# Performance work log

Measured on AMD Instinct MI355X. Metric: run time of the kernel, lower is better.

The kernel has to match this reference:

```python
import jax, jax.numpy as jnp
import numpy as np

MD = 4                  # corr_md
D = 2 * MD + 1          # patch_size = 9


def setup_inputs() -> dict:
    key = jax.random.key(0)
    k1, k2 = jax.random.split(key)
    b, c, h, w = 4, 128, 128, 256
    t1 = jax.random.normal(k1, (b, c, h, w), dtype=jnp.float32)
    t2 = jax.random.normal(k2, (b, c, h, w), dtype=jnp.float32)
    return {"t1": t1, "t2": t2}


def reference(t1, t2):
    # Local cost volume: for each displacement (di, dj) in [-MD, MD]^2,
    # out[b, p, y, x] = sum_c t1[b, c, y, x] * t2[b, c, y+di, x+dj]
    # with zero padding outside t2 (SpatialCorrelationSampler semantics,
    # kernel_size=1, stride=1, dilation_patch=1; no channel normalization).
    b, c, h, w = t1.shape
    t2p = jnp.pad(t2, ((0, 0), (0, 0), (MD, MD), (MD, MD)))
    # Loop over the fixed 9x9 displacement grid (81 small reductions);
    outs = [
        jnp.einsum('bchw,bchw->bhw', t1, t2p[:, :, i:i + h, j:j + w])
        for i in range(D) for j in range(D)
    ]
    return jnp.stack(outs, axis=1)  # [b, 81, h, w]
```

## Files before the change

### kernel.cpp

```cpp
#include <hip/hip_runtime.h>

#define NP 81
#define CC 128
#define HH 128
#define WW 256
#define SX 24
#define NXT 11
#define NBLK (NXT * 16 * 4)
#define YPAD 136
#define XPAD 272
#define WS_NEED (4ull * YPAD * XPAD * CC * 2ull)

typedef __attribute__((ext_vector_type(8))) short short8;
typedef __attribute__((ext_vector_type(4))) float f32x4;
typedef __attribute__((ext_vector_type(16))) float f32x16;

__device__ __forceinline__ short f2bf(float f) {
    unsigned int u = __builtin_bit_cast(unsigned int, f);
    u += 0x7fffu + ((u >> 16) & 1u);
    return (short)(u >> 16);
}

__global__ __launch_bounds__(256) void prepass_t2t(const float* __restrict__ t2,
                                                   short* __restrict__ ws) {
    const int blk = blockIdx.x;
    const int yp  = blk % YPAD;
    const int b   = blk / YPAD;
    const int tid = threadIdx.x;
    short* wrow = ws + (size_t)blk * XPAD * CC;
    const int y2 = yp - 4;
    const short8 z = {0, 0, 0, 0, 0, 0, 0, 0};
    if (y2 < 0 || y2 >= HH) {
        for (int u = tid; u < XPAD * CC / 8; u += 256)
            *(short8*)&wrow[(size_t)u * 8] = z;
        return;
    }
    __shared__ short sT[64 * 136];
    {
        const int xh = tid >> 4;
        const int xp = (xh < 4) ? xh : xh + 256;
        *(short8*)&wrow[(size_t)xp * CC + (tid & 15) * 8] = z;
    }
    const int c   = tid & 127;
    const int x4h = tid >> 7;
    const int oct = tid & 15;
    const int xr  = tid >> 4;
    const float* prow = t2 + ((size_t)(b * CC + c) * HH + y2) * WW;
    for (int ch = 0; ch < 4; ++ch) {
        const int xbase = ch * 64;
#pragma unroll
        for (int rr = 0; rr < 8; ++rr) {
            const int x4 = x4h + 2 * rr;
            const f32x4 vv = *(const f32x4*)&prow[xbase + x4 * 4];
#pragma unroll
            for (int j = 0; j < 4; ++j)
                sT[(x4 * 4 + j) * 136 + c] = f2bf(vv[j]);
        }
        __syncthreads();
#pragma unroll
        for (int r2 = 0; r2 < 4; ++r2) {
            const int x = xr + 16 * r2;
            const short8 vv = *(const short8*)&sT[x * 136 + oct * 8];
            *(short8*)&wrow[(size_t)(xbase + x + 4) * CC + oct * 8] = vv;
        }
        __syncthreads();
    }
}

__global__ __launch_bounds__(1024) void corr_main24(
        const float* __restrict__ t1, const short* __restrict__ ws,
        float* __restrict__ out) {
    const int bid = blockIdx.x;
    const int sw  = (bid & 7) * (NBLK / 8) + (bid >> 3);
    const int ys = sw & 15;
    const int v  = sw >> 4;
    const int xt = v % NXT;
    const int b  = v / NXT;
    const int X0 = xt * SX;
    const int y0 = ys * 8;

    const int tid  = threadIdx.x;
    const int lane = tid & 63;
    const int w    = tid >> 6;
    const int n    = lane & 31;
    const int g    = lane >> 5;

    __shared__ short sA[8 * SX * 128];
    __shared__ __align__(16) float obufs[16 * 9 * 28];

    const short* bp = ws + ((size_t)(b * YPAD + y0 + w) * XPAD + X0 + n) * CC
                    + g * 8;
    short8 bre[8];
#pragma unroll
    for (int kc = 0; kc < 8; ++kc)
        bre[kc] = *(const short8*)&bp[kc * 16];

#pragma unroll
    for (int i = 0; i < 6; ++i) {
        const int idx = tid + i * 1024;
        const int x4 = idx % 6;
        const int vv = idx / 6;
        const int c  = vv & 127;
        const int yy = vv >> 7;
        const int xg = X0 + x4 * 4;
        f32x4 t = {0.f, 0.f, 0.f, 0.f};
        if (xg < WW)
            t = *(const f32x4*)&t1[((size_t)(b * CC + c) * HH + y0 + yy) * WW + xg];
        const int oct = c >> 3;
#pragma unroll
        for (int j = 0; j < 4; ++j) {
            const int x = x4 * 4 + j;
            sA[yy * 3072 + x * 128 + ((oct ^ (x & 15)) * 8 + (c & 7))] = f2bf(t[j]);
        }
    }
    __syncthreads();

    const int ylo = (w > 8) ? (w - 8) : 0;
    const int yhi = (w < 7) ? w : 7;
    float* ob = &obufs[w * 252];

    for (int yy = ylo; yy <= yhi; ++yy) {
        const int sbase = yy * 3072 + n * 128;

        f32x16 a;
#pragma unroll
        for (int q = 0; q < 16; ++q) a[q] = 0.f;
#pragma unroll
        for (int kc = 0; kc < 8; ++kc) {
            const short8 af = *(const short8*)
                &sA[sbase + (((kc * 2 + g) ^ (n & 15)) * 8)];
            a = __builtin_amdgcn_mfma_f32_32x32x16_bf16(af, bre[kc], a, 0, 0, 0);
        }

#pragma unroll
        for (int q = 0; q < 16; ++q) {
            const int m  = (q & 3) + 8 * (q >> 2) + 4 * g;
            const int dj = n - m;
            if (dj >= 0 && dj <= 8 && m < SX) ob[dj * 28 + m] = a[q];
        }

        const int di = w - yy;
        const int y  = y0 + yy;
        if (lane < 54) {
            const int dj = lane / 6, xq = lane % 6;
            if (X0 + xq * 4 < WW) {
                f32x4 vv = *(const f32x4*)&ob[dj * 28 + xq * 4];
                *(f32x4*)&out[((size_t)(b * NP + di * 9 + dj) * HH + y) * WW
                              + X0 + xq * 4] = vv;
            }
        }
    }
}

__global__ __launch_bounds__(1024) void corr_fallback(
        const float* __restrict__ t1, const float* __restrict__ t2,
        float* __restrict__ out) {
    const int bid = blockIdx.x;
    const int sw  = (bid & 7) * (NBLK / 8) + (bid >> 3);
    const int ys = sw & 15;
    const int v  = sw >> 4;
    const int xt = v % NXT;
    const int b  = v / NXT;
    const int X0 = xt * SX;
    const int y0 = ys * 8;
    const int tid  = threadIdx.x;
    const int lane = tid & 63;
    const int w    = tid >> 6;
    const int n    = lane & 31;
    const int g    = lane >> 5;
    __shared__ short sA[8 * SX * 128];
    __shared__ __align__(16) float obufs[16 * 9 * 28];
    const size_t plane = (size_t)HH * WW;
    const int r = y0 - 4 + w;
#pragma unroll
    for (int i = 0; i < 3; ++i) {
        const int unit = tid + i * 1024;
        const int x    = unit % SX;
        const int rest = unit / SX;
        const int oct  = rest & 15;
        const int yy   = rest >> 4;
        short8 pk = {0,0,0,0,0,0,0,0};
        if (X0 + x < WW) {
            const float* p = t1 + ((size_t)(b * CC + oct * 8) * HH + (y0 + yy)) * WW
                           + X0 + x;
#pragma unroll
            for (int j = 0; j < 8; ++j) pk[j] = f2bf(p[(size_t)j * plane]);
        }
        *(short8*)&sA[yy * (SX * 128) + x * 128 + ((oct ^ (x & 15)) * 8)] = pk;
    }
    __syncthreads();
    const int x2 = X0 - 4 + n;
    const bool ok = (r >= 0) && (r < HH) && (x2 >= 0) && (x2 < WW);
    const int rc  = r  < 0 ? 0 : (r  > HH - 1 ? HH - 1 : r);
    const int xc  = x2 < 0 ? 0 : (x2 > WW - 1 ? WW - 1 : x2);
    const float* bp = t2 + ((size_t)(b * CC + g * 8) * HH + rc) * WW + xc;
    short8 bre[8];
#pragma unroll
    for (int kc = 0; kc < 8; ++kc) {
        short8 f;
#pragma unroll
        for (int j = 0; j < 8; ++j) f[j] = f2bf(bp[(size_t)(kc * 16 + j) * plane]);
        if (!ok) f = (short8){0,0,0,0,0,0,0,0};
        bre[kc] = f;
    }
    const int ylo = (w > 8) ? (w - 8) : 0;
    const int yhi = (w < 7) ? w : 7;
    float* ob = &obufs[w * 252];
    for (int yy = ylo; yy <= yhi; ++yy) {
        const int sbase = yy * (SX * 128) + n * 128;
        f32x16 a;
#pragma unroll
        for (int q = 0; q < 16; ++q) a[q] = 0.f;
#pragma unroll
        for (int kc = 0; kc < 8; ++kc) {
            const short8 af = *(const short8*)
                &sA[sbase + (((kc * 2 + g) ^ (n & 15)) * 8)];
            a = __builtin_amdgcn_mfma_f32_32x32x16_bf16(af, bre[kc], a, 0, 0, 0);
        }
#pragma unroll
        for (int q = 0; q < 16; ++q) {
            const int m  = (q & 3) + 8 * (q >> 2) + 4 * g;
            const int dj = n - m;
            if (dj >= 0 && dj <= 8 && m < SX) ob[dj * 28 + m] = a[q];
        }
        const int di = w - yy;
        const int y  = y0 + yy;
        if (lane < 54) {
            const int dj = lane / 6, xq = lane % 6;
            if (X0 + xq * 4 < WW) {
                f32x4 vv = *(const f32x4*)&ob[dj * 28 + xq * 4];
                *(f32x4*)&out[((size_t)(b * NP + di * 9 + dj) * HH + y) * WW
                              + X0 + xq * 4] = vv;
            }
        }
    }
}

extern "C" void kernel_launch(void* const* d_in, const int* in_sizes, int n_in,
                              void* d_out, int out_size, void* d_ws, size_t ws_size,
                              hipStream_t stream) {
    const float* t1 = (const float*)d_in[0];
    const float* t2 = (const float*)d_in[1];
    if (ws_size >= WS_NEED) {
        short* ws = (short*)d_ws;
        prepass_t2t<<<4 * YPAD, 256, 0, stream>>>(t2, ws);
        corr_main24<<<NBLK, 1024, 0, stream>>>(t1, ws, (float*)d_out);
    } else {
        corr_fallback<<<NBLK, 1024, 0, stream>>>(t1, t2, (float*)d_out);
    }
}
```

Measured before the change: 210.2 us.

## Shrink x-tile to 16, split prepass in halves, vectorize channel-packed loads

The main kernel moves from 24-wide x tiles (11 tiles, the last one partial) to 16-wide tiles, so there are exactly 1024 blocks and no bounds checks. This drops the wasted partial tile and the padding lanes in the MFMA M dimension, at the cost of more redundant loads of the halo t2 data per output. The t2 prepass now runs two blocks per row, each handling half the channels. It loads 8 channel planes directly and packs them into bf16 short8 without a shared-memory transpose. The t1 staging is likewise rewritten so each thread packs four channels into bf16x4 stores.

```diff
diff --git a/kernel.cpp b/kernel.cpp
--- a/kernel.cpp
+++ b/kernel.cpp
@@ -4,13 +4,14 @@
 #define CC 128
 #define HH 128
 #define WW 256
-#define SX 24
-#define NXT 11
-#define NBLK (NXT * 16 * 4)
 #define YPAD 136
 #define XPAD 272
 #define WS_NEED (4ull * YPAD * XPAD * CC * 2ull)
 
+#define SX 16
+#define NBLK 1024
+
+typedef __attribute__((ext_vector_type(4))) short bf16x4;
 typedef __attribute__((ext_vector_type(8))) short short8;
 typedef __attribute__((ext_vector_type(4))) float f32x4;
 typedef __attribute__((ext_vector_type(16))) float f32x16;
@@ -24,58 +25,52 @@
 __global__ __launch_bounds__(256) void prepass_t2t(const float* __restrict__ t2,
                                                    short* __restrict__ ws) {
     const int blk = blockIdx.x;
-    const int yp  = blk % YPAD;
-    const int b   = blk / YPAD;
+    const int hf  = blk & 1;
+    const int row = blk >> 1;
+    const int yp  = row % YPAD;
+    const int b   = row / YPAD;
     const int tid = threadIdx.x;
-    short* wrow = ws + (size_t)blk * XPAD * CC;
+    short* wrow = ws + (size_t)row * XPAD * CC;
     const int y2 = yp - 4;
-    const short8 z = {0, 0, 0, 0, 0, 0, 0, 0};
+    const short8 z = {0,0,0,0,0,0,0,0};
     if (y2 < 0 || y2 >= HH) {
-        for (int u = tid; u < XPAD * CC / 8; u += 256)
+        for (int u = tid + hf * 2176; u < 2176 + hf * 2176; u += 256)
             *(short8*)&wrow[(size_t)u * 8] = z;
         return;
     }
-    __shared__ short sT[64 * 136];
-    {
-        const int xh = tid >> 4;
-        const int xp = (xh < 4) ? xh : xh + 256;
+    if (tid < 128) {
+        const int idx = hf * 8 + (tid >> 4);
+        const int xp  = (idx < 4) ? idx : idx + 256;
         *(short8*)&wrow[(size_t)xp * CC + (tid & 15) * 8] = z;
     }
-    const int c   = tid & 127;
-    const int x4h = tid >> 7;
-    const int oct = tid & 15;
-    const int xr  = tid >> 4;
-    const float* prow = t2 + ((size_t)(b * CC + c) * HH + y2) * WW;
-    for (int ch = 0; ch < 4; ++ch) {
-        const int xbase = ch * 64;
-#pragma unroll
-        for (int rr = 0; rr < 8; ++rr) {
-            const int x4 = x4h + 2 * rr;
-            const f32x4 vv = *(const f32x4*)&prow[xbase + x4 * 4];
-#pragma unroll
-            for (int j = 0; j < 4; ++j)
-                sT[(x4 * 4 + j) * 136 + c] = f2bf(vv[j]);
-        }
-        __syncthreads();
-#pragma unroll
-        for (int r2 = 0; r2 < 4; ++r2) {
-            const int x = xr + 16 * r2;
-            const short8 vv = *(const short8*)&sT[x * 136 + oct * 8];
-            *(short8*)&wrow[(size_t)(xbase + x + 4) * CC + oct * 8] = vv;
-        }
-        __syncthreads();
-    }
-}
-
-__global__ __launch_bounds__(1024) void corr_main24(
+    const size_t plane = (size_t)HH * WW;
+#pragma unroll
+    for (int i = 0; i < 2; ++i) {
+        const int u   = tid + i * 256;
+        const int oct = hf * 8 + (u & 7);
+        const int xq  = u >> 3;
+        const float* p = t2 + ((size_t)(b * CC + oct * 8) * HH + y2) * WW + xq * 4;
+        f32x4 v[8];
+#pragma unroll
+        for (int j = 0; j < 8; ++j) v[j] = *(const f32x4*)&p[(size_t)j * plane];
+#pragma unroll
+        for (int jj = 0; jj < 4; ++jj) {
+            short8 s;
+#pragma unroll
+            for (int j = 0; j < 8; ++j) s[j] = f2bf(v[j][jj]);
+            *(short8*)&wrow[(size_t)(4 + xq * 4 + jj) * CC + oct * 8] = s;
+        }
+    }
+}
+
+__global__ __launch_bounds__(1024) void corr_main16(
         const float* __restrict__ t1, const short* __restrict__ ws,
         float* __restrict__ out) {
     const int bid = blockIdx.x;
     const int sw  = (bid & 7) * (NBLK / 8) + (bid >> 3);
-    const int ys = sw & 15;
-    const int v  = sw >> 4;
-    const int xt = v % NXT;
-    const int b  = v / NXT;
+    const int xt = sw & 15;
+    const int ys = (sw >> 4) & 15;
+    const int b  = sw >> 8;
     const int X0 = xt * SX;
     const int y0 = ys * 8;
 
@@ -86,7 +81,7 @@
     const int g    = lane >> 5;
 
     __shared__ short sA[8 * SX * 128];
-    __shared__ __align__(16) float obufs[16 * 9 * 28];
+    __shared__ __align__(16) float obufs[16 * 9 * 20];
 
     const short* bp = ws + ((size_t)(b * YPAD + y0 + w) * XPAD + X0 + n) * CC
                     + g * 8;
@@ -95,32 +90,37 @@
     for (int kc = 0; kc < 8; ++kc)
         bre[kc] = *(const short8*)&bp[kc * 16];
 
-#pragma unroll
-    for (int i = 0; i < 6; ++i) {
-        const int idx = tid + i * 1024;
-        const int x4 = idx % 6;
-        const int vv = idx / 6;
-        const int c  = vv & 127;
-        const int yy = vv >> 7;
-        const int xg = X0 + x4 * 4;
-        f32x4 t = {0.f, 0.f, 0.f, 0.f};
-        if (xg < WW)
-            t = *(const f32x4*)&t1[((size_t)(b * CC + c) * HH + y0 + yy) * WW + xg];
-        const int oct = c >> 3;
-#pragma unroll
-        for (int j = 0; j < 4; ++j) {
-            const int x = x4 * 4 + j;
-            sA[yy * 3072 + x * 128 + ((oct ^ (x & 15)) * 8 + (c & 7))] = f2bf(t[j]);
+    if (tid < 512) {
+        const int oct = tid & 15;
+        const int xq  = (tid >> 4) & 3;
+        const int yy  = tid >> 6;
+        const size_t plane = (size_t)HH * WW;
+        const float* p = t1 + ((size_t)(b * CC + oct * 8) * HH + y0 + yy) * WW
+                       + X0 + xq * 4;
+#pragma unroll
+        for (int h = 0; h < 2; ++h) {
+            f32x4 v[4];
+#pragma unroll
+            for (int j = 0; j < 4; ++j)
+                v[j] = *(const f32x4*)&p[(size_t)(h * 4 + j) * plane];
+#pragma unroll
+            for (int jj = 0; jj < 4; ++jj) {
+                const int x = xq * 4 + jj;
+                bf16x4 s;
+#pragma unroll
+                for (int j = 0; j < 4; ++j) s[j] = f2bf(v[j][jj]);
+                *(bf16x4*)&sA[yy * 2048 + x * 128 + ((oct ^ x) * 8) + h * 4] = s;
+            }
         }
     }
     __syncthreads();
 
     const int ylo = (w > 8) ? (w - 8) : 0;
     const int yhi = (w < 7) ? w : 7;
-    float* ob = &obufs[w * 252];
+    float* ob = &obufs[w * 180];
 
     for (int yy = ylo; yy <= yhi; ++yy) {
-        const int sbase = yy * 3072 + n * 128;
+        const int sbase = yy * 2048 + n * 128;
 
         f32x16 a;
 #pragma unroll
@@ -136,9 +136,94 @@
         for (int q = 0; q < 16; ++q) {
             const int m  = (q & 3) + 8 * (q >> 2) + 4 * g;
             const int dj = n - m;
-            if (dj >= 0 && dj <= 8 && m < SX) ob[dj * 28 + m] = a[q];
-        }
-
+            if (dj >= 0 && dj <= 8 && m < SX) ob[dj * 20 + m] = a[q];
+        }
+
+        const int di = w - yy;
+        const int y  = y0 + yy;
+        if (lane < 36) {
+            const int dj = lane >> 2, xq = lane & 3;
+            f32x4 vv = *(const f32x4*)&ob[dj * 20 + xq * 4];
+            *(f32x4*)&out[((size_t)(b * NP + di * 9 + dj) * HH + y) * WW
+                          + X0 + xq * 4] = vv;
+        }
+    }
+}
+
+#define FB_SX 24
+#define FB_NXT 11
+#define FB_NBLK (FB_NXT * 16 * 4)
+__global__ __launch_bounds__(1024) void corr_fallback(
+        const float* __restrict__ t1, const float* __restrict__ t2,
+        float* __restrict__ out) {
+    const int bid = blockIdx.x;
+    const int sw  = (bid & 7) * (FB_NBLK / 8) + (bid >> 3);
+    const int ys = sw & 15;
+    const int v  = sw >> 4;
+    const int xt = v % FB_NXT;
+    const int b  = v / FB_NXT;
+    const int X0 = xt * FB_SX;
+    const int y0 = ys * 8;
+    const int tid  = threadIdx.x;
+    const int lane = tid & 63;
+    const int w    = tid >> 6;
+    const int n    = lane & 31;
+    const int g    = lane >> 5;
+    __shared__ short sA[8 * FB_SX * 128];
+    __shared__ __align__(16) float obufs[16 * 9 * 28];
+    const size_t plane = (size_t)HH * WW;
+    const int r = y0 - 4 + w;
+#pragma unroll
+    for (int i = 0; i < 3; ++i) {
+        const int unit = tid + i * 1024;
+        const int x    = unit % FB_SX;
+        const int rest = unit / FB_SX;
+        const int oct  = rest & 15;
+        const int yy   = rest >> 4;
+        short8 pk = {0,0,0,0,0,0,0,0};
+        if (X0 + x < WW) {
+            const float* p = t1 + ((size_t)(b * CC + oct * 8) * HH + (y0 + yy)) * WW
+                           + X0 + x;
+#pragma unroll
+            for (int j = 0; j < 8; ++j) pk[j] = f2bf(p[(size_t)j * plane]);
+        }
+        *(short8*)&sA[yy * (FB_SX * 128) + x * 128 + ((oct ^ (x & 15)) * 8)] = pk;
+    }
+    __syncthreads();
+    const int x2 = X0 - 4 + n;
+    const bool ok = (r >= 0) && (r < HH) && (x2 >= 0) && (x2 < WW);
+    const int rc  = r  < 0 ? 0 : (r  > HH - 1 ? HH - 1 : r);
+    const int xc  = x2 < 0 ? 0 : (x2 > WW - 1 ? WW - 1 : x2);
+    const float* bp = t2 + ((size_t)(b * CC + g * 8) * HH + rc) * WW + xc;
+    short8 bre[8];
+#pragma unroll
+    for (int kc = 0; kc < 8; ++kc) {
+        short8 f;
+#pragma unroll
+        for (int j = 0; j < 8; ++j) f[j] = f2bf(bp[(size_t)(kc * 16 + j) * plane]);
+        if (!ok) f = (short8){0,0,0,0,0,0,0,0};
+        bre[kc] = f;
+    }
+    const int ylo = (w > 8) ? (w - 8) : 0;
+    const int yhi = (w < 7) ? w : 7;
+    float* ob = &obufs[w * 252];
+    for (int yy = ylo; yy <= yhi; ++yy) {
+        const int sbase = yy * (FB_SX * 128) + n * 128;
+        f32x16 a;
+#pragma unroll
+        for (int q = 0; q < 16; ++q) a[q] = 0.f;
+#pragma unroll
+        for (int kc = 0; kc < 8; ++kc) {
+            const short8 af = *(const short8*)
+                &sA[sbase + (((kc * 2 + g) ^ (n & 15)) * 8)];
+            a = __builtin_amdgcn_mfma_f32_32x32x16_bf16(af, bre[kc], a, 0, 0, 0);
+        }
+#pragma unroll
+        for (int q = 0; q < 16; ++q) {
+            const int m  = (q & 3) + 8 * (q >> 2) + 4 * g;
+            const int dj = n - m;
+            if (dj >= 0 && dj <= 8 && m < FB_SX) ob[dj * 28 + m] = a[q];
+        }
         const int di = w - yy;
         const int y  = y0 + yy;
         if (lane < 54) {
@@ -152,90 +237,6 @@
     }
 }
 
-__global__ __launch_bounds__(1024) void corr_fallback(
-        const float* __restrict__ t1, const float* __restrict__ t2,
-        float* __restrict__ out) {
-    const int bid = blockIdx.x;
-    const int sw  = (bid & 7) * (NBLK / 8) + (bid >> 3);
-    const int ys = sw & 15;
-    const int v  = sw >> 4;
-    const int xt = v % NXT;
-    const int b  = v / NXT;
-    const int X0 = xt * SX;
-    const int y0 = ys * 8;
-    const int tid  = threadIdx.x;
-    const int lane = tid & 63;
-    const int w    = tid >> 6;
-    const int n    = lane & 31;
-    const int g    = lane >> 5;
-    __shared__ short sA[8 * SX * 128];
-    __shared__ __align__(16) float obufs[16 * 9 * 28];
-    const size_t plane = (size_t)HH * WW;
-    const int r = y0 - 4 + w;
-#pragma unroll
-    for (int i = 0; i < 3; ++i) {
-        const int unit = tid + i * 1024;
-        const int x    = unit % SX;
-        const int rest = unit / SX;
-        const int oct  = rest & 15;
-        const int yy   = rest >> 4;
-        short8 pk = {0,0,0,0,0,0,0,0};
-        if (X0 + x < WW) {
-            const float* p = t1 + ((size_t)(b * CC + oct * 8) * HH + (y0 + yy)) * WW
-                           + X0 + x;
-#pragma unroll
-            for (int j = 0; j < 8; ++j) pk[j] = f2bf(p[(size_t)j * plane]);
-        }
-        *(short8*)&sA[yy * (SX * 128) + x * 128 + ((oct ^ (x & 15)) * 8)] = pk;
-    }
-    __syncthreads();
-    const int x2 = X0 - 4 + n;
-    const bool ok = (r >= 0) && (r < HH) && (x2 >= 0) && (x2 < WW);
-    const int rc  = r  < 0 ? 0 : (r  > HH - 1 ? HH - 1 : r);
-    const int xc  = x2 < 0 ? 0 : (x2 > WW - 1 ? WW - 1 : x2);
-    const float* bp = t2 + ((size_t)(b * CC + g * 8) * HH + rc) * WW + xc;
-    short8 bre[8];
-#pragma unroll
-    for (int kc = 0; kc < 8; ++kc) {
-        short8 f;
-#pragma unroll
-        for (int j = 0; j < 8; ++j) f[j] = f2bf(bp[(size_t)(kc * 16 + j) * plane]);
-        if (!ok) f = (short8){0,0,0,0,0,0,0,0};
-        bre[kc] = f;
-    }
-    const int ylo = (w > 8) ? (w - 8) : 0;
-    const int yhi = (w < 7) ? w : 7;
-    float* ob = &obufs[w * 252];
-    for (int yy = ylo; yy <= yhi; ++yy) {
-        const int sbase = yy * (SX * 128) + n * 128;
-        f32x16 a;
-#pragma unroll
-        for (int q = 0; q < 16; ++q) a[q] = 0.f;
-#pragma unroll
-        for (int kc = 0; kc < 8; ++kc) {
-            const short8 af = *(const short8*)
-                &sA[sbase + (((kc * 2 + g) ^ (n & 15)) * 8)];
-            a = __builtin_amdgcn_mfma_f32_32x32x16_bf16(af, bre[kc], a, 0, 0, 0);
-        }
-#pragma unroll
-        for (int q = 0; q < 16; ++q) {
-            const int m  = (q & 3) + 8 * (q >> 2) + 4 * g;
-            const int dj = n - m;
-            if (dj >= 0 && dj <= 8 && m < SX) ob[dj * 28 + m] = a[q];
-        }
-        const int di = w - yy;
-        const int y  = y0 + yy;
-        if (lane < 54) {
-            const int dj = lane / 6, xq = lane % 6;
-            if (X0 + xq * 4 < WW) {
-                f32x4 vv = *(const f32x4*)&ob[dj * 28 + xq * 4];
-                *(f32x4*)&out[((size_t)(b * NP + di * 9 + dj) * HH + y) * WW
-                              + X0 + xq * 4] = vv;
-            }
-        }
-    }
-}
-
 extern "C" void kernel_launch(void* const* d_in, const int* in_sizes, int n_in,
                               void* d_out, int out_size, void* d_ws, size_t ws_size,
                               hipStream_t stream) {
@@ -243,9 +244,9 @@
     const float* t2 = (const float*)d_in[1];
     if (ws_size >= WS_NEED) {
         short* ws = (short*)d_ws;
-        prepass_t2t<<<4 * YPAD, 256, 0, stream>>>(t2, ws);
-        corr_main24<<<NBLK, 1024, 0, stream>>>(t1, ws, (float*)d_out);
+        prepass_t2t<<<4 * YPAD * 2, 256, 0, stream>>>(t2, ws);
+        corr_main16<<<NBLK, 1024, 0, stream>>>(t1, ws, (float*)d_out);
     } else {
-        corr_fallback<<<NBLK, 1024, 0, stream>>>(t1, t2, (float*)d_out);
-    }
-}
+        corr_fallback<<<FB_NBLK, 1024, 0, stream>>>(t1, t2, (float*)d_out);
+    }
+}
```

After: 194.8 us. -7.3%, faster.
